# Optimization experiments

Measured on AMD Instinct MI355X. Metric: run time of the kernel, lower is better.

Reference implementation:

```python
import jax, jax.numpy as jnp
import numpy as np

B, N, C, H = 4, 2048, 1024, 16
D = C // H

def setup_inputs() -> dict:
    key = jax.random.key(0)
    k1, k2, k3 = jax.random.split(key, 3)
    x = jax.random.normal(k1, (B, N, C), dtype=jnp.float32)
    w_qkv = jax.random.normal(k2, (C, 3 * C), dtype=jnp.float32) * (C ** -0.5)
    w_proj = jax.random.normal(k3, (C, C), dtype=jnp.float32) * (C ** -0.5)
    b_proj = jnp.zeros((C,), dtype=jnp.float32)
    return {"x": x, "w_qkv": w_qkv, "w_proj": w_proj, "b_proj": b_proj}

def reference(x, w_qkv, w_proj, b_proj):
    scale = D ** -0.5
    qkv = x @ w_qkv                                   # [B,N,3C]
    qkv = qkv.reshape(B, N, 3, H, D).transpose(2, 0, 3, 1, 4)  # [3,B,H,N,D]
    q, k, v = qkv[0], qkv[1], qkv[2]
    attn = jnp.einsum('bhnd,bhmd->bhnm', q, k) * scale  # [B,H,N,N]
    attn = jax.nn.softmax(attn, axis=-1)
    o = jnp.einsum('bhnm,bhmd->bhnd', attn, v)          # [B,H,N,D]
    o = o.transpose(0, 2, 1, 3).reshape(B, N, C)
    return o @ w_proj + b_proj
```

## Files before the change

### kernel.cpp

```cpp
#include <hip/hip_runtime.h>
#include <hip/hip_bf16.h>


#define B_ 4
#define N_ 2048
#define C_ 1024
#define H_ 16
#define D_ 64
#define MCONST 24.0f

typedef __attribute__((ext_vector_type(8))) __bf16 bf16x8;
typedef __attribute__((ext_vector_type(4))) float f32x4;
typedef __attribute__((ext_vector_type(16))) float f32x16;
typedef unsigned int u32;
typedef __attribute__((ext_vector_type(4))) u32 u32x4;

__device__ inline unsigned short f2bf(float f) {
  __bf16 h = (__bf16)f;
  return __builtin_bit_cast(unsigned short, h);
}

__device__ __forceinline__ u32 pk2(float lo, float hi) {
  return (u32)f2bf(lo) | ((u32)f2bf(hi) << 16);
}

__device__ __forceinline__ void gld16(const void* g, void* l) {
  __builtin_amdgcn_global_load_lds(
      (const __attribute__((address_space(1))) u32*)g,
      (__attribute__((address_space(3))) u32*)l, 16, 0, 0);
}

__global__ __launch_bounds__(256) void cvt_bf16_kernel(
    const float* __restrict__ in, unsigned short* __restrict__ out) {
  int i = (blockIdx.x * 256 + threadIdx.x) * 8;
  float4 f0 = *(const float4*)&in[i];
  float4 f1 = *(const float4*)&in[i + 4];
  ushort4 h0, h1;
  h0.x = f2bf(f0.x); h0.y = f2bf(f0.y); h0.z = f2bf(f0.z); h0.w = f2bf(f0.w);
  h1.x = f2bf(f1.x); h1.y = f2bf(f1.y); h1.z = f2bf(f1.z); h1.w = f2bf(f1.w);
  *(ushort4*)&out[i] = h0;
  *(ushort4*)&out[i + 4] = h1;
}

__global__ __launch_bounds__(256) void transpose_cvt_kernel(
    const float* __restrict__ in, unsigned short* __restrict__ out,
    int K, int Nn) {
  __shared__ float tile[32][33];
  const int t = threadIdx.x;
  const int k0 = blockIdx.y * 32, n0 = blockIdx.x * 32;
  {
    int r = t >> 3, c = (t & 7) * 4;
    float4 f = *(const float4*)&in[(size_t)(k0 + r) * Nn + n0 + c];
    tile[r][c + 0] = f.x; tile[r][c + 1] = f.y;
    tile[r][c + 2] = f.z; tile[r][c + 3] = f.w;
  }
  __syncthreads();
  {
    int nr = t >> 3, kc = (t & 7) * 4;
    ushort4 h;
    h.x = f2bf(tile[kc + 0][nr]);
    h.y = f2bf(tile[kc + 1][nr]);
    h.z = f2bf(tile[kc + 2][nr]);
    h.w = f2bf(tile[kc + 3][nr]);
    *(ushort4*)&out[(size_t)(n0 + nr) * K + k0 + kc] = h;
  }
}

__global__ __launch_bounds__(256) void transpose_v_kernel(
    const unsigned short* __restrict__ vb, unsigned short* __restrict__ vtb) {
  __shared__ u32 tile[64][65];
  const int tid = threadIdx.x;
  const int n0 = blockIdx.x * 64;
  const int bh = blockIdx.y;
  const size_t base = (size_t)bh * N_ * D_;
#pragma unroll
  for (int i = 0; i < 2; i++) {
    int id = i * 256 + tid;
    int row = id >> 3, c8 = id & 7;
    uint4 v = *(const uint4*)&vb[base + (size_t)(n0 + row) * D_ + c8 * 8];
    const unsigned short* pv = (const unsigned short*)&v;
#pragma unroll
    for (int j = 0; j < 8; j++) tile[row][c8 * 8 + j] = pv[j];
  }
  __syncthreads();
#pragma unroll
  for (int i = 0; i < 2; i++) {
    int id = i * 256 + tid;
    int d = id >> 3, nc = id & 7;
    uint4 o;
    unsigned short* po = (unsigned short*)&o;
#pragma unroll
    for (int j = 0; j < 8; j++) po[j] = (unsigned short)tile[nc * 8 + j][d];
    *(uint4*)&vtb[base + (size_t)d * N_ + n0 + nc * 8] = o;
  }
}

template<int MODE>
__global__ __launch_bounds__(256) void gemm128_kernel(
    const unsigned short* __restrict__ A, const unsigned short* __restrict__ Bt,
    const float* __restrict__ bias,
    unsigned short* __restrict__ qb, unsigned short* __restrict__ kb,
    unsigned short* __restrict__ vb, float* __restrict__ outp,
    int M, int K, int Nout)
{
  __shared__ unsigned short Al[128 * 64];
  __shared__ unsigned short Bl[128 * 64];
  const int tid = threadIdx.x;
  const int w = tid >> 6, lane = tid & 63;
  const int l15 = lane & 15, lk = lane >> 4;
  const int wr = w >> 1, wc = w & 1;
  const int n0 = blockIdx.x * 128, m0 = blockIdx.y * 128;
  const int srow = tid >> 3;
  const int scol = (tid & 7) * 8;

  f32x4 acc[4][4];
#pragma unroll
  for (int m = 0; m < 4; m++)
#pragma unroll
    for (int n = 0; n < 4; n++) acc[m][n] = f32x4{0.f, 0.f, 0.f, 0.f};

  for (int kt = 0; kt < K; kt += 64) {
#pragma unroll
    for (int i = 0; i < 4; i++)
      gld16(&A[(size_t)(m0 + i * 32 + srow) * K + kt + scol],
            &Al[i * 2048 + w * 512]);
#pragma unroll
    for (int i = 0; i < 4; i++)
      gld16(&Bt[(size_t)(n0 + i * 32 + srow) * K + kt + scol],
            &Bl[i * 2048 + w * 512]);
    __syncthreads();

#pragma unroll
    for (int kk = 0; kk < 2; kk++) {
      bf16x8 af[4], bf[4];
#pragma unroll
      for (int m = 0; m < 4; m++)
        af[m] = *(const bf16x8*)&Al[(wr * 64 + m * 16 + l15) * 64 + kk * 32 + lk * 8];
#pragma unroll
      for (int n = 0; n < 4; n++)
        bf[n] = *(const bf16x8*)&Bl[(wc * 64 + n * 16 + l15) * 64 + kk * 32 + lk * 8];
#pragma unroll
      for (int m = 0; m < 4; m++)
#pragma unroll
        for (int n = 0; n < 4; n++)
          acc[m][n] = __builtin_amdgcn_mfma_f32_16x16x32_bf16(af[m], bf[n], acc[m][n], 0, 0, 0);
    }
    __syncthreads();
  }

  if (MODE == 0) {
#pragma unroll
    for (int n = 0; n < 4; n++) {
      int c = n0 + wc * 64 + n * 16 + l15;
      int tsel = c >> 10, h = (c >> 6) & 15, d = c & 63;
      unsigned short* dst = (tsel == 0) ? qb : (tsel == 1 ? kb : vb);
      float sc = (tsel == 0) ? 0.125f * 1.44269504088896340736f : 1.0f;
#pragma unroll
      for (int m = 0; m < 4; m++) {
#pragma unroll
        for (int r = 0; r < 4; r++) {
          int row = m0 + wr * 64 + m * 16 + lk * 4 + r;
          int b = row >> 11, nn = row & 2047;
          dst[(((size_t)(b * 16 + h)) * 2048 + nn) * 64 + d] = f2bf(acc[m][n][r] * sc);
        }
      }
    }
  } else {
#pragma unroll
    for (int n = 0; n < 4; n++) {
      int c = n0 + wc * 64 + n * 16 + l15;
      float bv = bias[c];
#pragma unroll
      for (int m = 0; m < 4; m++) {
#pragma unroll
        for (int r = 0; r < 4; r++) {
          int row = m0 + wr * 64 + m * 16 + lk * 4 + r;
          outp[(size_t)row * Nout + c] = acc[m][n][r] + bv;
        }
      }
    }
  }
}

__global__ __launch_bounds__(256) void flash_kernel(
    const unsigned short* __restrict__ qb, const unsigned short* __restrict__ kb,
    const unsigned short* __restrict__ vtb, unsigned short* __restrict__ ob)
{
  __shared__ unsigned short Kl[64 * 64];
  __shared__ unsigned short Vl[64 * 64];
  __shared__ float Lf[128];
  const int tid = threadIdx.x;
  const int w = tid >> 6;
  const int lane = tid & 63;
  const int l31 = lane & 31;
  const int hi = lane >> 5;
  const int q0 = blockIdx.x * 128;
  const int bh = blockIdx.y;
  const size_t base = (size_t)bh * N_ * D_;
  const unsigned short* Qg = qb + base;
  const unsigned short* Kg = kb + base;
  const unsigned short* Vtg = vtb + base;

  const int s_r = tid >> 3;
  const int s_sl = (tid & 7) ^ (s_r & 7);
  const int swz = (lane & 7) << 3;

  const int qrow_g = q0 + w * 32 + l31;
  bf16x8 qf[4];
#pragma unroll
  for (int ds = 0; ds < 4; ds++)
    qf[ds] = *(const bf16x8*)&Qg[(size_t)qrow_g * 64 + ds * 16 + hi * 8];

  f32x16 acc0, acc1, minit;
#pragma unroll
  for (int i = 0; i < 16; i++) { acc0[i] = 0.f; acc1[i] = 0.f; minit[i] = -MCONST; }
  float lrow = 0.f;

  for (int kv0 = 0; kv0 < N_; kv0 += 64) {
#pragma unroll
    for (int i = 0; i < 2; i++)
      gld16(&Kg[(size_t)(kv0 + i * 32 + s_r) * 64 + s_sl * 8],
            &Kl[i * 2048 + w * 512]);
#pragma unroll
    for (int i = 0; i < 2; i++)
      gld16(&Vtg[(size_t)(i * 32 + s_r) * N_ + kv0 + s_sl * 8],
            &Vl[i * 2048 + w * 512]);
    __syncthreads();

    u32 F[4][4];
#pragma unroll
    for (int t = 0; t < 2; t++) {
      f32x16 sa = minit;
      __builtin_amdgcn_s_setprio(1);
#pragma unroll
      for (int ds = 0; ds < 4; ds++) {
        bf16x8 a = *(const bf16x8*)&Kl[(t * 32 + l31) * 64 + ((ds * 16 + hi * 8) ^ swz)];
        sa = __builtin_amdgcn_mfma_f32_32x32x16_bf16(a, qf[ds], sa, 0, 0, 0);
      }
      __builtin_amdgcn_s_setprio(0);

      float p[16];
#pragma unroll
      for (int r = 0; r < 16; r++) p[r] = __builtin_amdgcn_exp2f(sa[r]);
      lrow += ((p[0] + p[1]) + (p[2] + p[3])) + ((p[4] + p[5]) + (p[6] + p[7]))
            + ((p[8] + p[9]) + (p[10] + p[11])) + ((p[12] + p[13]) + (p[14] + p[15]));

      u32 pk[8], sw[8];
#pragma unroll
      for (int j = 0; j < 8; j++) pk[j] = pk2(p[2 * j], p[2 * j + 1]);
#pragma unroll
      for (int j = 0; j < 8; j++) sw[j] = (u32)__shfl_xor((int)pk[j], 32);
      F[2 * t][0] = hi ? sw[2] : pk[0];
      F[2 * t][1] = hi ? sw[3] : pk[1];
      F[2 * t][2] = hi ? pk[2] : sw[0];
      F[2 * t][3] = hi ? pk[3] : sw[1];
      F[2 * t + 1][0] = hi ? sw[6] : pk[4];
      F[2 * t + 1][1] = hi ? sw[7] : pk[5];
      F[2 * t + 1][2] = hi ? pk[6] : sw[4];
      F[2 * t + 1][3] = hi ? pk[7] : sw[5];
    }

    __builtin_amdgcn_s_setprio(1);
#pragma unroll
    for (int ks = 0; ks < 4; ks++) {
      u32x4 fv = {F[ks][0], F[ks][1], F[ks][2], F[ks][3]};
      bf16x8 a = __builtin_bit_cast(bf16x8, fv);
      bf16x8 b0 = *(const bf16x8*)&Vl[(0 * 32 + l31) * 64 + ((ks * 16 + hi * 8) ^ swz)];
      acc0 = __builtin_amdgcn_mfma_f32_32x32x16_bf16(a, b0, acc0, 0, 0, 0);
      bf16x8 b1 = *(const bf16x8*)&Vl[(1 * 32 + l31) * 64 + ((ks * 16 + hi * 8) ^ swz)];
      acc1 = __builtin_amdgcn_mfma_f32_32x32x16_bf16(a, b1, acc1, 0, 0, 0);
    }
    __builtin_amdgcn_s_setprio(0);
    __syncthreads();
  }

  float rs = lrow + __shfl_xor(lrow, 32);
  if (lane < 32) Lf[w * 32 + l31] = rs;
  __syncthreads();

  const int b = bh >> 4, h = bh & 15;
#pragma unroll
  for (int r = 0; r < 16; r++) {
    int qr = (r & 3) + 8 * (r >> 2) + 4 * hi;
    float inv = 1.0f / Lf[w * 32 + qr];
    int nq = q0 + w * 32 + qr;
    size_t ob0 = (((size_t)b * N_ + nq) * H_ + h) * D_;
    ob[ob0 + l31]      = f2bf(acc0[r] * inv);
    ob[ob0 + 32 + l31] = f2bf(acc1[r] * inv);
  }
}

extern "C" void kernel_launch(void* const* d_in, const int* in_sizes, int n_in,
                              void* d_out, int out_size, void* d_ws, size_t ws_size,
                              hipStream_t stream) {
  const float* x      = (const float*)d_in[0];
  const float* w_qkv  = (const float*)d_in[1];
  const float* w_proj = (const float*)d_in[2];
  const float* b_proj = (const float*)d_in[3];
  float* out = (float*)d_out;

  const size_t qsz = (size_t)B_ * H_ * N_ * D_;
  unsigned short* qb     = (unsigned short*)d_ws;
  unsigned short* kb     = qb + qsz;
  unsigned short* vb     = kb + qsz;
  unsigned short* vtb    = vb + qsz;
  unsigned short* xbf    = vtb + qsz;
  unsigned short* ob     = xbf;
  unsigned short* wqkv_t = xbf + qsz;
  unsigned short* wproj_t= wqkv_t + (size_t)3072 * 1024;

  cvt_bf16_kernel<<<4096, 256, 0, stream>>>(x, xbf);
  transpose_cvt_kernel<<<dim3(3072 / 32, 1024 / 32), 256, 0, stream>>>(w_qkv, wqkv_t, 1024, 3072);
  transpose_cvt_kernel<<<dim3(1024 / 32, 1024 / 32), 256, 0, stream>>>(w_proj, wproj_t, 1024, 1024);

  gemm128_kernel<0><<<dim3(3072 / 128, 8192 / 128), 256, 0, stream>>>(
      xbf, wqkv_t, nullptr, qb, kb, vb, nullptr, 8192, 1024, 3072);

  transpose_v_kernel<<<dim3(N_ / 64, B_ * H_), 256, 0, stream>>>(vb, vtb);

  flash_kernel<<<dim3(N_ / 128, B_ * H_), 256, 0, stream>>>(qb, kb, vtb, ob);

  gemm128_kernel<1><<<dim3(1024 / 128, 8192 / 128), 256, 0, stream>>>(
      ob, wproj_t, b_proj, nullptr, nullptr, nullptr, out, 8192, 1024, 1024);
}
```

Before: 244.8 us.

## Split flash attention KV range across two wave groups and use permlane32 swap

The flash kernel now runs 512 threads per block. Two groups of four waves each process half of the KV sequence for the same 128 query rows, then combine partial outputs and row sums through shared memory before normalizing. The aim is to double the waves working on each query tile and so hide latency, since the grid only has 1024 blocks. It also replaces the shfl_xor-plus-select exchange of packed P fragments with permlane32_swap when that builtin exists. The cost is more LDS, extra block-wide syncs (both groups share one __syncthreads inside the loop), and a reduction epilogue.

```diff
diff --git a/kernel.cpp b/kernel.cpp
--- a/kernel.cpp
+++ b/kernel.cpp
@@ -13,6 +13,7 @@
 typedef __attribute__((ext_vector_type(4))) float f32x4;
 typedef __attribute__((ext_vector_type(16))) float f32x16;
 typedef unsigned int u32;
+typedef __attribute__((ext_vector_type(2))) u32 u32x2;
 typedef __attribute__((ext_vector_type(4))) u32 u32x4;
 
 __device__ inline unsigned short f2bf(float f) {
@@ -182,18 +183,21 @@
   }
 }
 
-__global__ __launch_bounds__(256) void flash_kernel(
+__global__ __launch_bounds__(512) void flash_kernel(
     const unsigned short* __restrict__ qb, const unsigned short* __restrict__ kb,
     const unsigned short* __restrict__ vtb, unsigned short* __restrict__ ob)
 {
-  __shared__ unsigned short Kl[64 * 64];
-  __shared__ unsigned short Vl[64 * 64];
-  __shared__ float Lf[128];
+  __shared__ unsigned short KVs[2][2][64 * 64];
+  __shared__ float Lf[2][128];
+  float* scratch = (float*)&KVs[0][0][0];
+
   const int tid = threadIdx.x;
   const int w = tid >> 6;
   const int lane = tid & 63;
   const int l31 = lane & 31;
   const int hi = lane >> 5;
+  const int g = w >> 2;
+  const int ws = w & 3;
   const int q0 = blockIdx.x * 128;
   const int bh = blockIdx.y;
   const size_t base = (size_t)bh * N_ * D_;
@@ -201,11 +205,14 @@
   const unsigned short* Kg = kb + base;
   const unsigned short* Vtg = vtb + base;
 
-  const int s_r = tid >> 3;
-  const int s_sl = (tid & 7) ^ (s_r & 7);
+  const int t8 = tid & 255;
+  const int s_r = t8 >> 3;
+  const int s_sl = (t8 & 7) ^ (s_r & 7);
   const int swz = (lane & 7) << 3;
-
-  const int qrow_g = q0 + w * 32 + l31;
+  unsigned short* Kl = &KVs[g][0][0];
+  unsigned short* Vl = &KVs[g][1][0];
+
+  const int qrow_g = q0 + ws * 32 + l31;
   bf16x8 qf[4];
 #pragma unroll
   for (int ds = 0; ds < 4; ds++)
@@ -216,15 +223,16 @@
   for (int i = 0; i < 16; i++) { acc0[i] = 0.f; acc1[i] = 0.f; minit[i] = -MCONST; }
   float lrow = 0.f;
 
-  for (int kv0 = 0; kv0 < N_; kv0 += 64) {
+  const int kvbeg = g * (N_ / 2);
+  for (int kv0 = kvbeg; kv0 < kvbeg + N_ / 2; kv0 += 64) {
 #pragma unroll
     for (int i = 0; i < 2; i++)
       gld16(&Kg[(size_t)(kv0 + i * 32 + s_r) * 64 + s_sl * 8],
-            &Kl[i * 2048 + w * 512]);
+            &Kl[i * 2048 + ws * 512]);
 #pragma unroll
     for (int i = 0; i < 2; i++)
       gld16(&Vtg[(size_t)(i * 32 + s_r) * N_ + kv0 + s_sl * 8],
-            &Vl[i * 2048 + w * 512]);
+            &Vl[i * 2048 + ws * 512]);
     __syncthreads();
 
     u32 F[4][4];
@@ -245,9 +253,20 @@
       lrow += ((p[0] + p[1]) + (p[2] + p[3])) + ((p[4] + p[5]) + (p[6] + p[7]))
             + ((p[8] + p[9]) + (p[10] + p[11])) + ((p[12] + p[13]) + (p[14] + p[15]));
 
-      u32 pk[8], sw[8];
+      u32 pk[8];
 #pragma unroll
       for (int j = 0; j < 8; j++) pk[j] = pk2(p[2 * j], p[2 * j + 1]);
+#if __has_builtin(__builtin_amdgcn_permlane32_swap)
+      u32x2 r02 = __builtin_amdgcn_permlane32_swap(pk[0], pk[2], false, false);
+      u32x2 r13 = __builtin_amdgcn_permlane32_swap(pk[1], pk[3], false, false);
+      u32x2 r46 = __builtin_amdgcn_permlane32_swap(pk[4], pk[6], false, false);
+      u32x2 r57 = __builtin_amdgcn_permlane32_swap(pk[5], pk[7], false, false);
+      F[2 * t][0] = r02[0]; F[2 * t][2] = r02[1];
+      F[2 * t][1] = r13[0]; F[2 * t][3] = r13[1];
+      F[2 * t + 1][0] = r46[0]; F[2 * t + 1][2] = r46[1];
+      F[2 * t + 1][1] = r57[0]; F[2 * t + 1][3] = r57[1];
+#else
+      u32 sw[8];
 #pragma unroll
       for (int j = 0; j < 8; j++) sw[j] = (u32)__shfl_xor((int)pk[j], 32);
       F[2 * t][0] = hi ? sw[2] : pk[0];
@@ -258,6 +277,7 @@
       F[2 * t + 1][1] = hi ? sw[7] : pk[5];
       F[2 * t + 1][2] = hi ? pk[6] : sw[4];
       F[2 * t + 1][3] = hi ? pk[7] : sw[5];
+#endif
     }
 
     __builtin_amdgcn_s_setprio(1);
@@ -275,18 +295,31 @@
   }
 
   float rs = lrow + __shfl_xor(lrow, 32);
-  if (lane < 32) Lf[w * 32 + l31] = rs;
+  if (lane < 32) Lf[g][ws * 32 + l31] = rs;
   __syncthreads();
 
-  const int b = bh >> 4, h = bh & 15;
-#pragma unroll
-  for (int r = 0; r < 16; r++) {
-    int qr = (r & 3) + 8 * (r >> 2) + 4 * hi;
-    float inv = 1.0f / Lf[w * 32 + qr];
-    int nq = q0 + w * 32 + qr;
-    size_t ob0 = (((size_t)b * N_ + nq) * H_ + h) * D_;
-    ob[ob0 + l31]      = f2bf(acc0[r] * inv);
-    ob[ob0 + 32 + l31] = f2bf(acc1[r] * inv);
+  if (g == 0) {
+#pragma unroll
+    for (int r = 0; r < 16; r++) {
+      int qr = (r & 3) + 8 * (r >> 2) + 4 * hi;
+      scratch[(ws * 32 + qr) * 64 + l31]      = acc0[r];
+      scratch[(ws * 32 + qr) * 64 + 32 + l31] = acc1[r];
+    }
+  }
+  __syncthreads();
+  if (g == 1) {
+    const int b = bh >> 4, h = bh & 15;
+#pragma unroll
+    for (int r = 0; r < 16; r++) {
+      int qr = (r & 3) + 8 * (r >> 2) + 4 * hi;
+      float inv = 1.0f / (Lf[0][ws * 32 + qr] + Lf[1][ws * 32 + qr]);
+      float o0 = scratch[(ws * 32 + qr) * 64 + l31]      + acc0[r];
+      float o1 = scratch[(ws * 32 + qr) * 64 + 32 + l31] + acc1[r];
+      int nq = q0 + ws * 32 + qr;
+      size_t ob0 = (((size_t)b * N_ + nq) * H_ + h) * D_;
+      ob[ob0 + l31]      = f2bf(o0 * inv);
+      ob[ob0 + 32 + l31] = f2bf(o1 * inv);
+    }
   }
 }
 
@@ -318,7 +351,7 @@
 
   transpose_v_kernel<<<dim3(N_ / 64, B_ * H_), 256, 0, stream>>>(vb, vtb);
 
-  flash_kernel<<<dim3(N_ / 128, B_ * H_), 256, 0, stream>>>(qb, kb, vtb, ob);
+  flash_kernel<<<dim3(N_ / 128, B_ * H_), 512, 0, stream>>>(qb, kb, vtb, ob);
 
   gemm128_kernel<1><<<dim3(1024 / 128, 8192 / 128), 256, 0, stream>>>(
       ob, wproj_t, b_proj, nullptr, nullptr, nullptr, out, 8192, 1024, 1024);
```

New measurement: 223.2 us. 1.1x faster.
